# Optimization experiments

Hardware: AMD Instinct MI355X
Metric: run time of the kernel (lower is better)

Reference implementation:

```python
import jax, jax.numpy as jnp
import numpy as np

N_HEADS = 16
EPS = 1e-5

def _ln(h, g, b):
    mu = jnp.mean(h, axis=-1, keepdims=True)
    var = jnp.var(h, axis=-1, keepdims=True)
    return (h - mu) * jax.lax.rsqrt(var + EPS) * g + b

def setup_inputs() -> dict:
    key = jax.random.key(0)
    ks = jax.random.split(key, 8)
    B, S, D, M = 2, 2048, 2048, 8192
    x = jax.random.normal(ks[0], (B, S, D), dtype=jnp.float32)
    # causal mask: True where attention is disallowed (j > i)
    mask = jnp.triu(jnp.ones((S, S), dtype=bool), k=1)[None, None]
    s = 1.0 / np.sqrt(D)
    Wq = jax.random.normal(ks[1], (D, D), dtype=jnp.float32) * s
    Wk = jax.random.normal(ks[2], (D, D), dtype=jnp.float32) * s
    Wv = jax.random.normal(ks[3], (D, D), dtype=jnp.float32) * s
    Wo = jax.random.normal(ks[4], (D, D), dtype=jnp.float32) * s
    W1 = jax.random.normal(ks[5], (D, M), dtype=jnp.float32) * s
    b1 = jnp.zeros((M,), dtype=jnp.float32)
    W2 = jax.random.normal(ks[6], (M, D), dtype=jnp.float32) * (1.0 / np.sqrt(M))
    b2 = jnp.zeros((D,), dtype=jnp.float32)
    ln1_g = jnp.ones((D,), jnp.float32); ln1_b = jnp.zeros((D,), jnp.float32)
    ln2_g = jnp.ones((D,), jnp.float32); ln2_b = jnp.zeros((D,), jnp.float32)
    return dict(x=x, self_attn_mask=mask, Wq=Wq, Wk=Wk, Wv=Wv, Wo=Wo,
                ln1_g=ln1_g, ln1_b=ln1_b, W1=W1, b1=b1, W2=W2, b2=b2,
                ln2_g=ln2_g, ln2_b=ln2_b)

def reference(x, self_attn_mask, Wq, Wk, Wv, Wo, ln1_g, ln1_b, W1, b1, W2, b2, ln2_g, ln2_b):
    B, S, D = x.shape
    n = N_HEADS
    d = D // n
    # --- self-attention with pre-norm residual ---
    h = _ln(x, ln1_g, ln1_b)
    # NOTE: source uses .view(b, n_heads, i, head_dim) with NO transpose -> plain reshape
    q = (h @ Wq).reshape(B, n, S, d)
    k = (h @ Wk).reshape(B, n, S, d)
    v = (h @ Wv).reshape(B, n, S, d)
    score = jnp.einsum('bnid,bnjd->bnij', q, k)
    # NOTE: source masks BEFORE scaling, so -1e9 is also divided by sqrt(d)
    score = jnp.where(self_attn_mask, jnp.float32(-1e9), score) / jnp.sqrt(jnp.float32(d))
    w = jax.nn.softmax(score, axis=3)
    o = jnp.einsum('bnij,bnjd->bnid', w, v)
    o = o.transpose(0, 2, 1, 3).reshape(B, S, D)  # b n i d -> b i (n d)
    x = x + o @ Wo
    # --- FFN with pre-norm residual ---
    h2 = _ln(x, ln2_g, ln2_b)
    ff = jnp.maximum(h2 @ W1 + b1, 0.0) @ W2 + b2
    return x + ff
```

## Files before the change

kernel.cpp:

```cpp
#include <hip/hip_runtime.h>
#include <cstdint>

using bf16x8 = __attribute__((ext_vector_type(8))) short;
using f32x4  = __attribute__((ext_vector_type(4))) float;

__device__ __forceinline__ unsigned short f2bf(float f) {
  union { float f; unsigned u; } v; v.f = f;
  unsigned u = v.u;
  u += 0x7fffu + ((u >> 16) & 1u);
  return (unsigned short)(u >> 16);
}
__device__ __forceinline__ float bf2f(unsigned short s) {
  union { unsigned u; float f; } v; v.u = ((unsigned)s) << 16; return v.f;
}

__device__ __forceinline__ void gload_lds16(const unsigned short* g, unsigned short* l) {
  __builtin_amdgcn_global_load_lds(
      (const __attribute__((address_space(1))) unsigned int*)g,
      (__attribute__((address_space(3))) unsigned int*)l, 16, 0, 0);
}

__global__ __launch_bounds__(256) void ln_kernel(
    const float* __restrict__ x, const float* __restrict__ g,
    const float* __restrict__ bb, unsigned short* __restrict__ h)
{
  const int D = 2048;
  const int row = blockIdx.x;
  const float* xr = x + (size_t)row * D;
  const int t = threadIdx.x;
  float4 v0 = ((const float4*)xr)[t];
  float4 v1 = ((const float4*)xr)[t + 256];
  float s  = v0.x+v0.y+v0.z+v0.w + v1.x+v1.y+v1.z+v1.w;
  float ss = v0.x*v0.x+v0.y*v0.y+v0.z*v0.z+v0.w*v0.w
           + v1.x*v1.x+v1.y*v1.y+v1.z*v1.z+v1.w*v1.w;
  #pragma unroll
  for (int off = 1; off < 64; off <<= 1) {
    s  += __shfl_xor(s, off);
    ss += __shfl_xor(ss, off);
  }
  __shared__ float red[8];
  const int wave = t >> 6, lane = t & 63;
  if (lane == 0) { red[wave] = s; red[4+wave] = ss; }
  __syncthreads();
  s  = red[0]+red[1]+red[2]+red[3];
  ss = red[4]+red[5]+red[6]+red[7];
  const float mu   = s * (1.f/2048.f);
  const float var  = ss * (1.f/2048.f) - mu*mu;
  const float rstd = rsqrtf(var + 1e-5f);
  unsigned short* hr = h + (size_t)row * D;
  #pragma unroll
  for (int q = 0; q < 2; ++q) {
    float4 v = q ? v1 : v0;
    int vecidx = t + q*256;
    float4 gg  = ((const float4*)g)[vecidx];
    float4 bv  = ((const float4*)bb)[vecidx];
    ushort4 o;
    o.x = f2bf((v.x-mu)*rstd*gg.x + bv.x);
    o.y = f2bf((v.y-mu)*rstd*gg.y + bv.y);
    o.z = f2bf((v.z-mu)*rstd*gg.z + bv.z);
    o.w = f2bf((v.w-mu)*rstd*gg.w + bv.w);
    *(ushort4*)(hr + vecidx*4) = o;
  }
}

__global__ __launch_bounds__(256) void transpose_cast(
    const float* __restrict__ W, unsigned short* __restrict__ WT,
    int K, int N)
{
  __shared__ float tile[32][33];
  const int tx = threadIdx.x, ty = threadIdx.y;
  const int n0 = blockIdx.x * 32, k0 = blockIdx.y * 32;
  #pragma unroll
  for (int r = 0; r < 4; ++r)
    tile[ty + r*8][tx] = W[(size_t)(k0 + ty + r*8) * N + n0 + tx];
  __syncthreads();
  #pragma unroll
  for (int r = 0; r < 4; ++r)
    WT[(size_t)(n0 + ty + r*8) * K + k0 + tx] = f2bf(tile[tx][ty + r*8]);
}

template<bool BIAS>
__global__ __launch_bounds__(256) void reduce_splitk(
    const unsigned short* __restrict__ P, const float* __restrict__ resid,
    const float* __restrict__ bias, float* __restrict__ out)
{
  const size_t MN8 = (size_t)4096 * 2048 / 8;
  for (size_t i = (size_t)blockIdx.x * 256 + threadIdx.x; i < MN8;
       i += (size_t)gridDim.x * 256) {
    bf16x8 p0 = ((const bf16x8*)P)[i];
    bf16x8 p1 = ((const bf16x8*)P)[i + MN8];
    float4 r0 = ((const float4*)resid)[i*2];
    float4 r1 = ((const float4*)resid)[i*2 + 1];
    float4 b0 = {}, b1 = {};
    if (BIAS) {
      b0 = ((const float4*)bias)[(i & 255) * 2];
      b1 = ((const float4*)bias)[(i & 255) * 2 + 1];
    }
    float4 o0, o1;
    o0.x = bf2f((unsigned short)p0[0]) + bf2f((unsigned short)p1[0]) + r0.x + b0.x;
    o0.y = bf2f((unsigned short)p0[1]) + bf2f((unsigned short)p1[1]) + r0.y + b0.y;
    o0.z = bf2f((unsigned short)p0[2]) + bf2f((unsigned short)p1[2]) + r0.z + b0.z;
    o0.w = bf2f((unsigned short)p0[3]) + bf2f((unsigned short)p1[3]) + r0.w + b0.w;
    o1.x = bf2f((unsigned short)p0[4]) + bf2f((unsigned short)p1[4]) + r1.x + b1.x;
    o1.y = bf2f((unsigned short)p0[5]) + bf2f((unsigned short)p1[5]) + r1.y + b1.y;
    o1.z = bf2f((unsigned short)p0[6]) + bf2f((unsigned short)p1[6]) + r1.z + b1.z;
    o1.w = bf2f((unsigned short)p0[7]) + bf2f((unsigned short)p1[7]) + r1.w + b1.w;
    ((float4*)out)[i*2]     = o0;
    ((float4*)out)[i*2 + 1] = o1;
  }
}

template<bool BIAS, bool RELU, bool RESID, bool OUTBF16>
__global__ __launch_bounds__(512, 2) void gemm9(
    const unsigned short* __restrict__ A, const unsigned short* __restrict__ BT,
    const float* __restrict__ bias, const float* __restrict__ resid,
    void* __restrict__ Cp, int M, int N, int K, int kdepth, int nbx, int ntiles)
{
  constexpr int BM = 256, BN = 256, BK = 64;
  __shared__ __align__(16) unsigned short lds[2][(BM + BN) * BK];

  const int tid  = threadIdx.x;
  const int lane = tid & 63, wave = tid >> 6;
  const int l15 = lane & 15, lh = lane >> 4;
  const int wr = wave >> 2, wc = wave & 3;

  const int nwg = gridDim.x, q8 = nwg >> 3, wg = blockIdx.x;
  const int swz = (wg & 7) * q8 + (wg >> 3);
  const int split = swz / ntiles;
  const int tile  = swz % ntiles;
  const size_t bm = (size_t)(tile / nbx) * BM;
  const size_t bn = (size_t)(tile % nbx) * BN;
  A  += (size_t)split * kdepth;
  BT += (size_t)split * kdepth;
  const int nk = kdepth >> 6;

  const int srow = tid >> 3;
  const int sc   = (tid & 7) ^ (srow & 7);
  const unsigned short* aSrc = A  + (bm + srow) * (size_t)K + sc * 8;
  const unsigned short* bSrc = BT + (bn + srow) * (size_t)K + sc * 8;
  const size_t qStride = (size_t)64 * K;

  const int aswz = (l15 & 7) << 4;
  const int rx0 = (lh * 16) ^ aswz;
  const int rx1 = (64 + lh * 16) ^ aswz;
  char* const lbase = (char*)&lds[0][0];

  bf16x8 af[4][2][2];
  bf16x8 bfr[2][4];
  f32x4  acc[8][4] = {};

  auto stA = [&](int buf, int kt2, int qq) {
    gload_lds16(aSrc + (size_t)kt2 * BK + qq * qStride,
                &lds[buf][qq * 4096 + tid * 8]);
  };
  auto stB = [&](int buf, int kt2, int qq) {
    gload_lds16(bSrc + (size_t)kt2 * BK + qq * qStride,
                &lds[buf][BM * BK + qq * 4096 + tid * 8]);
  };
  auto rdA4 = [&](int buf, int q, int slot) {
    const char* p = lbase + buf * 65536 + (wr*32 + l15) * 128 + q * 8192;
    #pragma unroll
    for (int mi = 0; mi < 2; ++mi) {
      af[slot][mi][0] = *(const bf16x8*)(p + mi*2048 + rx0);
      af[slot][mi][1] = *(const bf16x8*)(p + mi*2048 + rx1);
    }
  };
  auto rdB8 = [&](int buf) {
    const char* p = lbase + buf * 65536 + 32768 + (wc*64 + l15) * 128;
    #pragma unroll
    for (int n = 0; n < 4; ++n) {
      bfr[0][n] = *(const bf16x8*)(p + n*2048 + rx0);
      bfr[1][n] = *(const bf16x8*)(p + n*2048 + rx1);
    }
  };

#define CLUSTER(P)                                                         \
  __builtin_amdgcn_s_setprio(1);                                           \
  { _Pragma("unroll")                                                      \
    for (int mi = 0; mi < 2; ++mi)                                         \
      { _Pragma("unroll")                                                  \
        for (int n = 0; n < 4; ++n)                                        \
          { _Pragma("unroll")                                              \
            for (int kk = 0; kk < 2; ++kk)                                 \
              acc[(P)*2+mi][n] = __builtin_amdgcn_mfma_f32_16x16x32_bf16(  \
                  af[P][mi][kk], bfr[kk][n], acc[(P)*2+mi][n], 0, 0, 0);   \
          } } }                                                            \
  __builtin_amdgcn_s_setprio(0);
#define BAR() asm volatile("" ::: "memory"); __builtin_amdgcn_s_barrier(); \
              asm volatile("" ::: "memory")

  #pragma unroll
  for (int qq = 0; qq < 4; ++qq) stB(0, 0, qq);
  #pragma unroll
  for (int qq = 0; qq < 4; ++qq) stA(0, 0, qq);
  #pragma unroll
  for (int qq = 0; qq < 4; ++qq) stB(1, 1, qq);
  #pragma unroll
  for (int qq = 0; qq < 4; ++qq) stA(1, 1, qq);
  asm volatile("s_waitcnt vmcnt(1)" ::: "memory");
  BAR();
  rdA4(0, 0, 0); rdA4(0, 1, 1); rdB8(0);
  BAR();

  for (int kt = 0; kt < nk; ++kt) {
    const int buf = kt & 1, nb = buf ^ 1;
    const bool hasNext = (kt + 1 < nk);
    const bool pf = (kt + 2 < nk);
    if (kt > 0) {
      asm volatile("s_waitcnt vmcnt(1)" ::: "memory");
      BAR();
    }
    if (pf) { stB(buf, kt+2, 0); stB(buf, kt+2, 1); stA(buf, kt+2, 0); }
    rdA4(buf, 2, 2);
    __builtin_amdgcn_sched_barrier(0);
    CLUSTER(0);
    BAR();
    if (pf) { stB(buf, kt+2, 2); stB(buf, kt+2, 3); stA(buf, kt+2, 1); stA(buf, kt+2, 2); }
    rdA4(buf, 3, 3);
    __builtin_amdgcn_sched_barrier(0);
    CLUSTER(1);
    BAR();
    if (pf) { stA(buf, kt+2, 3); }
    if (hasNext) rdA4(nb, 0, 0);
    __builtin_amdgcn_sched_barrier(0);
    CLUSTER(2);
    BAR();
    if (hasNext) rdA4(nb, 1, 1);
    __builtin_amdgcn_sched_barrier(0);
    CLUSTER(3);
    if (hasNext) rdB8(nb);
  }
#undef CLUSTER
#undef BAR

  float bv[4];
  if (BIAS) {
    #pragma unroll
    for (int n = 0; n < 4; ++n) bv[n] = bias[bn + wc*64 + n*16 + l15];
  }
  unsigned short* Cb = (unsigned short*)Cp + (size_t)split * M * N;
  float*          Cf = (float*)Cp + (size_t)split * M * N;
  #pragma unroll
  for (int p = 0; p < 4; ++p) {
    #pragma unroll
    for (int mi = 0; mi < 2; ++mi) {
      #pragma unroll
      for (int r = 0; r < 4; ++r) {
        size_t rrow = bm + (size_t)(p*4 + wr*2 + mi)*16 + lh*4 + r;
        #pragma unroll
        for (int n = 0; n < 4; ++n) {
          size_t ccol = bn + wc*64 + n*16 + l15;
          float v = acc[p*2+mi][n][r];
          if (BIAS)  v += bv[n];
          if (RELU)  v = fmaxf(v, 0.f);
          if (RESID) v += resid[rrow*(size_t)N + ccol];
          if (OUTBF16) Cb[rrow*(size_t)N + ccol] = f2bf(v);
          else         Cf[rrow*(size_t)N + ccol] = v;
        }
      }
    }
  }
}

__global__ __launch_bounds__(256) void attn_kernel(
    const unsigned short* __restrict__ QKV, unsigned short* __restrict__ O)
{
  constexpr float SCALE = 0.08838834764831845f;
  __shared__ __align__(16) unsigned short Kl[64*128];
  __shared__ __align__(16) unsigned short Vf[64*128];
  __shared__ __align__(16) unsigned short Pl[4*1024];
  const int bid = blockIdx.x;
  const int qt = 31 - (bid >> 5);
  const int nh = bid & 15;
  const int b  = (bid >> 4) & 1;
  const int t = threadIdx.x;
  const int lane = t & 63, wave = t >> 6;
  const int l15 = lane & 15, lh = lane >> 4;
  const int i0 = qt*64 + wave*16;
  const size_t RS = 6144;
  const size_t base = (size_t)b * 2048 * RS;

  const unsigned short* qrow = QKV + base + (size_t)(nh*128 + (i0 >> 4)) * RS;
  bf16x8 qf[4];
  #pragma unroll
  for (int c = 0; c < 4; ++c)
    qf[c] = *(const bf16x8*)(qrow + l15*128 + c*32 + lh*8);

  f32x4 of[8] = {};
  float mrun[4], lrun[4];
  #pragma unroll
  for (int r = 0; r < 4; ++r) { mrun[r] = -INFINITY; lrun[r] = 0.f; }

  const int nkt = qt + 1;
  bf16x8 kr[4], vr[4];
  auto loadKV = [&](int kt) {
    #pragma unroll
    for (int q = 0; q < 4; ++q) {
      int c = t + q*256;
      int j = c >> 4, dd0 = (c & 15) * 8;
      const size_t grow = base + (size_t)(nh*128 + kt*4 + (j >> 4)) * RS + (j & 15)*128 + dd0;
      kr[q] = *(const bf16x8*)(QKV + grow + 2048);
      vr[q] = *(const bf16x8*)(QKV + grow + 4096);
    }
  };
  loadKV(0);

  for (int kt = 0; kt < nkt; ++kt) {
    __syncthreads();
    #pragma unroll
    for (int q = 0; q < 4; ++q) {
      int c = t + q*256;
      int j = c >> 4, dd0 = (c & 15) * 8;
      *(bf16x8*)((char*)Kl + ((j*256 + dd0*2) ^ ((j & 7) << 4))) = kr[q];
      int ks = j >> 5, jq = j & 31;
      int cc = dd0 >> 4;
      int wb = ks*8192 + cc*1024 + (((dd0 & 15) + 16*((jq >> 3) & 3)) & ~7)*16 + (jq & 7)*2;
      #pragma unroll
      for (int e = 0; e < 8; ++e)
        *(unsigned short*)((char*)Vf + wb + ((e ^ cc) * 16)) = (unsigned short)vr[q][e];
    }
    __syncthreads();
    if (kt + 1 < nkt) loadKV(kt + 1);

    f32x4 sc[4] = {};
    #pragma unroll
    for (int jt = 0; jt < 4; ++jt) {
      int row = jt*16 + l15;
      const char* kb = (const char*)Kl + row*256;
      const int sw = (row & 7) << 4;
      #pragma unroll
      for (int c = 0; c < 4; ++c) {
        bf16x8 kf = *(const bf16x8*)(kb + ((c*64 + lh*16) ^ sw));
        sc[jt] = __builtin_amdgcn_mfma_f32_16x16x32_bf16(qf[c], kf, sc[jt], 0, 0, 0);
      }
    }

    float fac[4];
    char* pw = (char*)Pl + wave*2048;
    #pragma unroll
    for (int r = 0; r < 4; ++r) {
      float s0 = sc[0][r]*SCALE, s1 = sc[1][r]*SCALE, s2 = sc[2][r]*SCALE, s3 = sc[3][r]*SCALE;
      if (kt == qt) {
        const int i = i0 + lh*4 + r;
        const int j = kt*64 + l15;
        s0 = (j      > i) ? -INFINITY : s0;
        s1 = (j + 16 > i) ? -INFINITY : s1;
        s2 = (j + 32 > i) ? -INFINITY : s2;
        s3 = (j + 48 > i) ? -INFINITY : s3;
      }
      float mx = fmaxf(fmaxf(s0, s1), fmaxf(s2, s3));
      #pragma unroll
      for (int mk = 1; mk < 16; mk <<= 1) mx = fmaxf(mx, __shfl_xor(mx, mk));
      const float mnew = fmaxf(mrun[r], mx);
      float p0 = __expf(s0 - mnew), p1 = __expf(s1 - mnew);
      float p2 = __expf(s2 - mnew), p3 = __expf(s3 - mnew);
      float psum = (p0 + p1) + (p2 + p3);
      #pragma unroll
      for (int mk = 1; mk < 16; mk <<= 1) psum += __shfl_xor(psum, mk);
      fac[r]  = __expf(mrun[r] - mnew);
      lrun[r] = lrun[r]*fac[r] + psum;
      mrun[r] = mnew;
      const int io = lh*4 + r;
      const int swp = (io & 7) << 4;
      char* pr = pw + io*128;
      *(unsigned short*)(pr + ((     l15*2) ^ swp)) = f2bf(p0);
      *(unsigned short*)(pr + ((32 + l15*2) ^ swp)) = f2bf(p1);
      *(unsigned short*)(pr + ((64 + l15*2) ^ swp)) = f2bf(p2);
      *(unsigned short*)(pr + ((96 + l15*2) ^ swp)) = f2bf(p3);
    }
    #pragma unroll
    for (int c = 0; c < 8; ++c)
      #pragma unroll
      for (int r = 0; r < 4; ++r)
        of[c][r] *= fac[r];

    const char* prd = pw + l15*128;
    const int psw = (l15 & 7) << 4;
    bf16x8 pa0 = *(const bf16x8*)(prd + ((     lh*16) ^ psw));
    bf16x8 pa1 = *(const bf16x8*)(prd + ((64 + lh*16) ^ psw));

    #pragma unroll
    for (int c = 0; c < 8; ++c) {
      const char* vb = (const char*)Vf + c*1024 + ((lane ^ c) * 16);
      bf16x8 v0 = *(const bf16x8*)(vb);
      bf16x8 v1 = *(const bf16x8*)(vb + 8192);
      of[c] = __builtin_amdgcn_mfma_f32_16x16x32_bf16(pa0, v0, of[c], 0, 0, 0);
      of[c] = __builtin_amdgcn_mfma_f32_16x16x32_bf16(pa1, v1, of[c], 0, 0, 0);
    }
  }

  unsigned short* orow = O + ((size_t)(b*2048 + i0))*2048 + nh*128;
  #pragma unroll
  for (int r = 0; r < 4; ++r) {
    const float inv = 1.f / lrun[r];
    #pragma unroll
    for (int c = 0; c < 8; ++c)
      orow[(size_t)(lh*4 + r)*2048 + c*16 + l15] = f2bf(of[c][r]*inv);
  }
}

extern "C" void kernel_launch(void* const* d_in, const int* in_sizes, int n_in,
                              void* d_out, int out_size, void* d_ws, size_t ws_size,
                              hipStream_t stream)
{
  const float* x    = (const float*)d_in[0];
  const float* Wq   = (const float*)d_in[2];
  const float* Wk   = (const float*)d_in[3];
  const float* Wv   = (const float*)d_in[4];
  const float* Wo   = (const float*)d_in[5];
  const float* ln1g = (const float*)d_in[6];
  const float* ln1b = (const float*)d_in[7];
  const float* W1   = (const float*)d_in[8];
  const float* b1   = (const float*)d_in[9];
  const float* W2   = (const float*)d_in[10];
  const float* b2   = (const float*)d_in[11];
  const float* ln2g = (const float*)d_in[12];
  const float* ln2b = (const float*)d_in[13];
  float* out = (float*)d_out;

  char* ws = (char*)d_ws;
  unsigned short* WqkvT  = (unsigned short*)(ws);
  unsigned short* WoT    = (unsigned short*)(ws + 25165824);
  unsigned short* W1T    = (unsigned short*)(ws + 33554432);
  unsigned short* W2T    = (unsigned short*)(ws + 67108864);
  unsigned short* h      = (unsigned short*)(ws + 100663296);
  float*          x2     = (float*)(ws + 117440512);
  unsigned short* QKV    = (unsigned short*)(ws + 150994944);
  unsigned short* attn_o = (unsigned short*)(ws + 201326592);
  unsigned short* ff1    = (unsigned short*)(ws + 150994944);
  unsigned short* Pwo    = (unsigned short*)(ws + 150994944);
  unsigned short* Pw2    = (unsigned short*)(ws);

  dim3 tb(32, 8);
  transpose_cast<<<dim3(64, 64),  tb, 0, stream>>>(Wq, WqkvT,                2048, 2048);
  transpose_cast<<<dim3(64, 64),  tb, 0, stream>>>(Wk, WqkvT + 2048*2048,    2048, 2048);
  transpose_cast<<<dim3(64, 64),  tb, 0, stream>>>(Wv, WqkvT + 2*2048*2048,  2048, 2048);
  transpose_cast<<<dim3(64, 64),  tb, 0, stream>>>(Wo, WoT,                  2048, 2048);
  transpose_cast<<<dim3(256, 64), tb, 0, stream>>>(W1, W1T,                  2048, 8192);
  transpose_cast<<<dim3(64, 256), tb, 0, stream>>>(W2, W2T,                  8192, 2048);

  ln_kernel<<<4096, 256, 0, stream>>>(x, ln1g, ln1b, h);
  gemm9<false,false,false,true><<<384, 512, 0, stream>>>(
      h, WqkvT, nullptr, nullptr, QKV, 4096, 6144, 2048, 2048, 24, 384);
  attn_kernel<<<1024, 256, 0, stream>>>(QKV, attn_o);
  gemm9<false,false,false,true><<<256, 512, 0, stream>>>(
      attn_o, WoT, nullptr, nullptr, Pwo, 4096, 2048, 2048, 1024, 8, 128);
  reduce_splitk<false><<<2048, 256, 0, stream>>>(Pwo, x, nullptr, x2);
  ln_kernel<<<4096, 256, 0, stream>>>(x2, ln2g, ln2b, h);
  gemm9<true,true,false,true><<<512, 512, 0, stream>>>(
      h, W1T, b1, nullptr, ff1, 4096, 8192, 2048, 2048, 32, 512);
  gemm9<false,false,false,true><<<256, 512, 0, stream>>>(
      ff1, W2T, nullptr, nullptr, Pw2, 4096, 2048, 8192, 4096, 8, 128);
  reduce_splitk<true><<<2048, 256, 0, stream>>>(Pw2, x2, b2, out);
}
```

Baseline: 624.3 us.

## Rework GEMM pipeline to stream A fragments per cluster and reorder prefetch

The GEMM main loop is restructured so each wave reads only the A fragment for the current MFMA cluster instead of holding four slots, and the wave-to-row mapping changes so each wave owns a contiguous 128-row band. Global-to-LDS prefetch is now issued in finer quarters interleaved across the four clusters, with explicit vmcnt/lgkmcnt waits and barriers per cluster. The aim is to cut register pressure from the A fragment array and to spread memory traffic more evenly against compute. In exchange it adds more barriers and full LDS waits per iteration, which could expose LDS latency that the old code hid.

```diff
diff --git a/kernel.cpp b/kernel.cpp
--- a/kernel.cpp
+++ b/kernel.cpp
@@ -111,7 +111,7 @@
 }
 
 template<bool BIAS, bool RELU, bool RESID, bool OUTBF16>
-__global__ __launch_bounds__(512, 2) void gemm9(
+__global__ __launch_bounds__(512, 2) void gemm10(
     const unsigned short* __restrict__ A, const unsigned short* __restrict__ BT,
     const float* __restrict__ bias, const float* __restrict__ resid,
     void* __restrict__ Cp, int M, int N, int K, int kdepth, int nbx, int ntiles)
@@ -145,7 +145,7 @@
   const int rx1 = (64 + lh * 16) ^ aswz;
   char* const lbase = (char*)&lds[0][0];
 
-  bf16x8 af[4][2][2];
+  bf16x8 af[2][2];
   bf16x8 bfr[2][4];
   f32x4  acc[8][4] = {};
 
@@ -157,13 +157,13 @@
     gload_lds16(bSrc + (size_t)kt2 * BK + qq * qStride,
                 &lds[buf][BM * BK + qq * 4096 + tid * 8]);
   };
-  auto rdA4 = [&](int buf, int q, int slot) {
-    const char* p = lbase + buf * 65536 + (wr*32 + l15) * 128 + q * 8192;
-    #pragma unroll
-    for (int mi = 0; mi < 2; ++mi) {
-      af[slot][mi][0] = *(const bf16x8*)(p + mi*2048 + rx0);
-      af[slot][mi][1] = *(const bf16x8*)(p + mi*2048 + rx1);
-    }
+  auto rdA = [&](int buf, int p) {
+    const char* pa = lbase + buf * 65536 + (wr*2 + (p >> 1)) * 8192
+                   + ((p & 1) * 32 + l15) * 128;
+    af[0][0] = *(const bf16x8*)(pa + rx0);
+    af[0][1] = *(const bf16x8*)(pa + rx1);
+    af[1][0] = *(const bf16x8*)(pa + 2048 + rx0);
+    af[1][1] = *(const bf16x8*)(pa + 2048 + rx1);
   };
   auto rdB8 = [&](int buf) {
     const char* p = lbase + buf * 65536 + 32768 + (wc*64 + l15) * 128;
@@ -183,55 +183,59 @@
           { _Pragma("unroll")                                              \
             for (int kk = 0; kk < 2; ++kk)                                 \
               acc[(P)*2+mi][n] = __builtin_amdgcn_mfma_f32_16x16x32_bf16(  \
-                  af[P][mi][kk], bfr[kk][n], acc[(P)*2+mi][n], 0, 0, 0);   \
+                  af[mi][kk], bfr[kk][n], acc[(P)*2+mi][n], 0, 0, 0);      \
           } } }                                                            \
   __builtin_amdgcn_s_setprio(0);
 #define BAR() asm volatile("" ::: "memory"); __builtin_amdgcn_s_barrier(); \
               asm volatile("" ::: "memory")
-
-  #pragma unroll
-  for (int qq = 0; qq < 4; ++qq) stB(0, 0, qq);
-  #pragma unroll
-  for (int qq = 0; qq < 4; ++qq) stA(0, 0, qq);
-  #pragma unroll
-  for (int qq = 0; qq < 4; ++qq) stB(1, 1, qq);
-  #pragma unroll
-  for (int qq = 0; qq < 4; ++qq) stA(1, 1, qq);
-  asm volatile("s_waitcnt vmcnt(1)" ::: "memory");
-  BAR();
-  rdA4(0, 0, 0); rdA4(0, 1, 1); rdB8(0);
+#define WAITL0() asm volatile("s_waitcnt lgkmcnt(0)" ::: "memory");        \
+                 __builtin_amdgcn_sched_barrier(0)
+
+  stB(0,0,0); stB(0,0,1); stB(0,0,2); stB(0,0,3);
+  stA(0,0,0); stA(0,0,2); stA(0,0,1); stA(0,0,3);
+  if (nk > 1) {
+    stB(1,1,0); stB(1,1,1); stB(1,1,2); stB(1,1,3);
+    stA(1,1,0); stA(1,1,2);
+    asm volatile("s_waitcnt vmcnt(6)" ::: "memory");
+  } else {
+    asm volatile("s_waitcnt vmcnt(0)" ::: "memory");
+  }
   BAR();
 
   for (int kt = 0; kt < nk; ++kt) {
     const int buf = kt & 1, nb = buf ^ 1;
-    const bool hasNext = (kt + 1 < nk);
     const bool pf = (kt + 2 < nk);
-    if (kt > 0) {
-      asm volatile("s_waitcnt vmcnt(1)" ::: "memory");
-      BAR();
-    }
-    if (pf) { stB(buf, kt+2, 0); stB(buf, kt+2, 1); stA(buf, kt+2, 0); }
-    rdA4(buf, 2, 2);
-    __builtin_amdgcn_sched_barrier(0);
+    rdA(buf, 0); rdB8(buf);
+    if (kt + 1 < nk) { stA(nb, kt+1, 1); stA(nb, kt+1, 3); }
+    asm volatile("s_waitcnt lgkmcnt(8)" ::: "memory");
+    BAR();
+    WAITL0();
     CLUSTER(0);
     BAR();
-    if (pf) { stB(buf, kt+2, 2); stB(buf, kt+2, 3); stA(buf, kt+2, 1); stA(buf, kt+2, 2); }
-    rdA4(buf, 3, 3);
-    __builtin_amdgcn_sched_barrier(0);
+    rdA(buf, 1);
+    if (pf) { stB(buf, kt+2, 0); stB(buf, kt+2, 1); }
+    asm volatile("s_waitcnt vmcnt(10)" ::: "memory");
+    BAR();
+    WAITL0();
     CLUSTER(1);
     BAR();
-    if (pf) { stA(buf, kt+2, 3); }
-    if (hasNext) rdA4(nb, 0, 0);
-    __builtin_amdgcn_sched_barrier(0);
+    rdA(buf, 2);
+    if (pf) { stB(buf, kt+2, 2); stB(buf, kt+2, 3); }
+    BAR();
+    WAITL0();
     CLUSTER(2);
     BAR();
-    if (hasNext) rdA4(nb, 1, 1);
-    __builtin_amdgcn_sched_barrier(0);
+    rdA(buf, 3);
+    if (pf) { stA(buf, kt+2, 0); stA(buf, kt+2, 2); }
+    asm volatile("s_waitcnt vmcnt(8)" ::: "memory");
+    BAR();
+    WAITL0();
     CLUSTER(3);
-    if (hasNext) rdB8(nb);
+    BAR();
   }
 #undef CLUSTER
 #undef BAR
+#undef WAITL0
 
   float bv[4];
   if (BIAS) {
@@ -246,7 +250,7 @@
     for (int mi = 0; mi < 2; ++mi) {
       #pragma unroll
       for (int r = 0; r < 4; ++r) {
-        size_t rrow = bm + (size_t)(p*4 + wr*2 + mi)*16 + lh*4 + r;
+        size_t rrow = bm + (size_t)wr*128 + p*32 + mi*16 + lh*4 + r;
         #pragma unroll
         for (int n = 0; n < 4; ++n) {
           size_t ccol = bn + wc*64 + n*16 + l15;
@@ -440,16 +444,16 @@
   transpose_cast<<<dim3(64, 256), tb, 0, stream>>>(W2, W2T,                  8192, 2048);
 
   ln_kernel<<<4096, 256, 0, stream>>>(x, ln1g, ln1b, h);
-  gemm9<false,false,false,true><<<384, 512, 0, stream>>>(
+  gemm10<false,false,false,true><<<384, 512, 0, stream>>>(
       h, WqkvT, nullptr, nullptr, QKV, 4096, 6144, 2048, 2048, 24, 384);
   attn_kernel<<<1024, 256, 0, stream>>>(QKV, attn_o);
-  gemm9<false,false,false,true><<<256, 512, 0, stream>>>(
+  gemm10<false,false,false,true><<<256, 512, 0, stream>>>(
       attn_o, WoT, nullptr, nullptr, Pwo, 4096, 2048, 2048, 1024, 8, 128);
   reduce_splitk<false><<<2048, 256, 0, stream>>>(Pwo, x, nullptr, x2);
   ln_kernel<<<4096, 256, 0, stream>>>(x2, ln2g, ln2b, h);
-  gemm9<true,true,false,true><<<512, 512, 0, stream>>>(
+  gemm10<true,true,false,true><<<512, 512, 0, stream>>>(
       h, W1T, b1, nullptr, ff1, 4096, 8192, 2048, 2048, 32, 512);
-  gemm9<false,false,false,true><<<256, 512, 0, stream>>>(
+  gemm10<false,false,false,true><<<256, 512, 0, stream>>>(
       ff1, W2T, nullptr, nullptr, Pw2, 4096, 2048, 8192, 4096, 8, 128);
   reduce_splitk<true><<<2048, 256, 0, stream>>>(Pw2, x2, b2, out);
 }
```

After: 632.0 us. About the same (+1.2%).
